# Performance work log

Hardware: AMD Instinct MI355X
Metric: run time of the kernel (lower is better)

Reference implementation:

```python
import jax, jax.numpy as jnp
import numpy as np

D = 256      # input_dim (object feature dim)
H = 256      # hidden_dim
N0 = 4096    # nodes in frame 0
N1 = 4096    # nodes in frame 1
E = 131072   # edges
MP_ITER = 3
LN_EPS = 1e-5


def _glorot(k, shape):
    return jax.random.normal(k, shape, jnp.float32) * (1.0 / np.sqrt(shape[0]))


def setup_inputs() -> dict:
    key = jax.random.key(0)
    ks = jax.random.split(key, 20)
    z = lambda n: jnp.zeros((n,), jnp.float32)
    o = lambda n: jnp.ones((n,), jnp.float32)
    return {
        'node0': jax.random.normal(ks[0], (N0, D), jnp.float32),
        'node1': jax.random.normal(ks[1], (N1, D), jnp.float32),
        'row': jax.random.randint(ks[2], (E,), 0, N0, jnp.int32),
        'col': jax.random.randint(ks[3], (E,), 0, N1, jnp.int32),
        # edge_mlp: Linear(2D,H) ReLU Linear(H,H) LN ReLU Linear(H,H)
        'e_w1': _glorot(ks[4], (2 * D, H)), 'e_b1': z(H),
        'e_w2': _glorot(ks[5], (H, H)),     'e_b2': z(H),
        'e_g': o(H), 'e_be': z(H),
        'e_w3': _glorot(ks[6], (H, H)),     'e_b3': z(H),
        # node_mlp: Linear(H+D,H) ReLU Linear(H,H) LN ReLU Linear(H,D)
        'n_w1': _glorot(ks[7], (H + D, H)), 'n_b1': z(H),
        'n_w2': _glorot(ks[8], (H, H)),     'n_b2': z(H),
        'n_g': o(H), 'n_be': z(H),
        'n_w3': _glorot(ks[9], (H, D)),     'n_b3': z(D),
        # edge_predictor: Linear(2D,H) ReLU Linear(H,1)
        'p_w1': _glorot(ks[10], (2 * D, H)), 'p_b1': z(H),
        'p_w2': _glorot(ks[11], (H, 1)),     'p_b2': z(1),
    }


def _ln(x, g, b):
    mu = jnp.mean(x, axis=-1, keepdims=True)
    var = jnp.mean(jnp.square(x - mu), axis=-1, keepdims=True)
    return (x - mu) * jax.lax.rsqrt(var + LN_EPS) * g + b


def reference(node0, node1, row, col,
              e_w1, e_b1, e_w2, e_b2, e_g, e_be, e_w3, e_b3,
              n_w1, n_b1, n_w2, n_b2, n_g, n_be, n_w3, n_b3,
              p_w1, p_b1, p_w2, p_b2):
    def edge_mlp(x):
        h = jax.nn.relu(x @ e_w1 + e_b1)
        h = _ln(h @ e_w2 + e_b2, e_g, e_be)
        return jax.nn.relu(h) @ e_w3 + e_b3

    def node_mlp(x):
        h = jax.nn.relu(x @ n_w1 + n_b1)
        h = _ln(h @ n_w2 + n_b2, n_g, n_be)
        return jax.nn.relu(h) @ n_w3 + n_b3

    for _ in range(MP_ITER):
        # gather -> edge MLP -> scatter-add -> node MLP (+ residual)
        e_in = jnp.concatenate([node0[row], node1[col]], axis=1)  # [E, 2D]
        edge_attr = edge_mlp(e_in)                                 # [E, H]
        agg = jax.ops.segment_sum(edge_attr, row, num_segments=node0.shape[0])  # [N0, H]
        node0 = node_mlp(jnp.concatenate([node0, agg], axis=1)) + node0

    pred_in = jnp.concatenate([node0[row], node1[col]], axis=1)   # [E, 2D]
    h = jax.nn.relu(pred_in @ p_w1 + p_b1)
    edge_preds = jax.nn.sigmoid(h @ p_w2 + p_b2)                   # [E, 1]
    return edge_preds
```

## Files before the change

### kernel.cpp

```cpp
#include <hip/hip_runtime.h>
#include <hip/hip_bf16.h>

#define NN0 4096
#define NEDGE 131072
#define NMP 3

typedef __attribute__((ext_vector_type(8))) short bf16x8;
typedef __attribute__((ext_vector_type(4))) float f32x4;

__device__ __forceinline__ unsigned short f2b(float v) {
  __hip_bfloat16 h = __float2bfloat16(v);
  return __builtin_bit_cast(unsigned short, h);
}

__device__ __forceinline__ float b2f(short s) {
  return __builtin_bit_cast(float, ((unsigned)(unsigned short)s) << 16);
}

__device__ __forceinline__ void gload_lds16(const void* g, void* l) {
  __builtin_amdgcn_global_load_lds(
      (const __attribute__((address_space(1))) void*)g,
      (__attribute__((address_space(3))) void*)l, 16, 0, 0);
}

#define MFMA(a, b, c) __builtin_amdgcn_mfma_f32_16x16x32_bf16((a), (b), (c), 0, 0, 0)

__device__ __forceinline__ void wfrag_body(const float* __restrict__ src,
                                           unsigned short* __restrict__ dst,
                                           int t, int C, int lgnkt) {
  const int j = t & 7;
  const int l = (t >> 3) & 63;
  const int rest = t >> 9;
  const int kt = rest & ((1 << lgnkt) - 1);
  const int ct = rest >> lgnkt;
  const int r = l & 15, q = l >> 4;
  const int k = (kt << 5) + (q << 3) + j;
  const int c = (ct << 4) + r;
  dst[t] = f2b(src[k * C + c]);
}

__global__ void prep_kernel(
    const float* e1, const float* e2, const float* e3,
    const float* n1, const float* n2, const float* n3, const float* p1,
    unsigned short* We1, unsigned short* We2, unsigned short* We3,
    unsigned short* Wn1, unsigned short* Wn2, unsigned short* Wn3,
    unsigned short* Wp1,
    const float* __restrict__ node0, const float* __restrict__ node1,
    unsigned short* __restrict__ n0b, float* __restrict__ n0f,
    unsigned short* __restrict__ n1b,
    const int* __restrict__ rowi, int* __restrict__ counts) {
  const int b = blockIdx.x;
  const int tid = threadIdx.x;
  if (b < 512)       wfrag_body(e1, We1, (b - 0) * 256 + tid, 256, 4);
  else if (b < 768)  wfrag_body(e2, We2, (b - 512) * 256 + tid, 256, 3);
  else if (b < 1024) wfrag_body(e3, We3, (b - 768) * 256 + tid, 256, 3);
  else if (b < 1536) wfrag_body(n1, Wn1, (b - 1024) * 256 + tid, 256, 4);
  else if (b < 1792) wfrag_body(n2, Wn2, (b - 1536) * 256 + tid, 256, 3);
  else if (b < 2048) wfrag_body(n3, Wn3, (b - 1792) * 256 + tid, 256, 3);
  else if (b < 2560) wfrag_body(p1, Wp1, (b - 2048) * 256 + tid, 256, 4);
  else {
    const int t = (b - 2560) * 256 + tid;
    const float a = node0[t], v = node1[t];
    n0b[t] = f2b(a);
    n0f[t] = a;
    n1b[t] = f2b(v);
    if (t < NEDGE) atomicAdd(&counts[rowi[t]], 1);
  }
}

__global__ void scan_kernel(const int* __restrict__ counts, int* __restrict__ pos) {
  __shared__ int part[256];
  const int t = threadIdx.x;
  const int base = t << 4;
  int local[16];
  int s = 0;
  #pragma unroll
  for (int i = 0; i < 16; ++i) { local[i] = s; s += counts[base + i]; }
  part[t] = s;
  __syncthreads();
  int val = s;
  #pragma unroll
  for (int off = 1; off < 256; off <<= 1) {
    const int add = (t >= off) ? part[t - off] : 0;
    __syncthreads();
    val += add;
    part[t] = val;
    __syncthreads();
  }
  const int excl = val - s;
  #pragma unroll
  for (int i = 0; i < 16; ++i) pos[base + i] = excl + local[i];
}

__global__ void fill_kernel(const int* __restrict__ rowi, int* __restrict__ pos,
                            int* __restrict__ perm) {
  const int e = blockIdx.x * 256 + threadIdx.x;
  if (e < NEDGE) {
    const int slot = atomicAdd(&pos[rowi[e]], 1);
    perm[slot] = e;
  }
}

__global__ __launch_bounds__(256, 2) void pre_gemm_kernel(
    const unsigned short* __restrict__ n0bA, const unsigned short* __restrict__ n1b,
    const unsigned short* __restrict__ We1, const unsigned short* __restrict__ Wp1,
    const float* __restrict__ e_b1,
    unsigned short* __restrict__ P0, unsigned short* __restrict__ P1,
    unsigned short* __restrict__ Pp1)
{
  __shared__ unsigned short smem[32 * 256];
  const int b = blockIdx.x;
  const int grp = b >> 7, mb = b & 127;
  const unsigned short* A;
  const unsigned short* W;
  int ktoff;
  const float* bias;
  unsigned short* out;
  if (grp == 0)      { A = n0bA; W = We1; ktoff = 0; bias = e_b1;    out = P0;  }
  else if (grp == 1) { A = n1b;  W = We1; ktoff = 8; bias = nullptr; out = P1;  }
  else               { A = n1b;  W = Wp1; ktoff = 8; bias = nullptr; out = Pp1; }

  const int tid = (int)threadIdx.x;
  const int ww = tid >> 6, l = tid & 63, r = l & 15, q = l >> 4;
  const int c0 = ww << 6;
  const int swz = (r & 7) << 4;

  #pragma unroll
  for (int s = 0; s < 4; ++s) {
    const int rp = (ww << 3) + (s << 1);
    const int row = rp + (l >> 5);
    const int g = (l & 31) ^ (row & 7);
    gload_lds16(A + (mb * 32 + row) * 256 + g * 8, &smem[rp * 256]);
  }
  __syncthreads();

  f32x4 acc[2][4];
  #pragma unroll
  for (int mt = 0; mt < 2; ++mt)
    #pragma unroll
    for (int nt = 0; nt < 4; ++nt)
      acc[mt][nt] = f32x4{0.f, 0.f, 0.f, 0.f};

  for (int ks = 0; ks < 8; ++ks) {
    bf16x8 a[2];
    #pragma unroll
    for (int mt = 0; mt < 2; ++mt)
      a[mt] = *(const bf16x8*)((const char*)smem + ((mt << 4) + r) * 512 +
                               (((ks << 6) | (q << 4)) ^ swz));
    #pragma unroll
    for (int nt = 0; nt < 4; ++nt) {
      bf16x8 bfr = *(const bf16x8*)(W + ((((ww << 2) + nt) << 4) + ktoff + ks) * 512 + (l << 3));
      #pragma unroll
      for (int mt = 0; mt < 2; ++mt)
        acc[mt][nt] = MFMA(a[mt], bfr, acc[mt][nt]);
    }
  }
  #pragma unroll
  for (int nt = 0; nt < 4; ++nt) {
    const int col = c0 + (nt << 4) + r;
    const float bv = bias ? bias[col] : 0.f;
    #pragma unroll
    for (int mt = 0; mt < 2; ++mt)
      #pragma unroll
      for (int i = 0; i < 4; ++i)
        out[(mb * 32 + (mt << 4) + (q << 2) + i) * 256 + col] = f2b(acc[mt][nt][i] + bv);
  }
}

__global__ __launch_bounds__(256, 2) void edge_mlp_kernel(
    const unsigned short* __restrict__ P0b, const unsigned short* __restrict__ P1b,
    const int* __restrict__ rowi, const int* __restrict__ coli,
    const int* __restrict__ perm,
    const unsigned short* __restrict__ W2, const float* __restrict__ b2,
    const float* __restrict__ lng, const float* __restrict__ lnb,
    float* __restrict__ S)
{
  __shared__ unsigned short smem[64 * 256];
  __shared__ float lnp[512];
  __shared__ int rs_s[64];
  __shared__ unsigned long long bmask_s;

  const int tid = (int)threadIdx.x;
  const int wn = tid >> 6, l = tid & 63, r = l & 15, q = l >> 4;
  const int bid = (int)blockIdx.x;
  const int swzb = ((bid & 7) << 8) + (bid >> 3);
  const int e0 = swzb * 64;
  const int c0 = wn << 6;
  const int swz = (r & 7) << 4;

  const int hrow = tid >> 2;
  const int cq = tid & 3;
  const int pe = perm[e0 + hrow];
  const int mrow = rowi[pe], mcol = coli[pe];
  if (cq == 0) rs_s[hrow] = mrow;
  const unsigned short* pu = P0b + mrow * 256;
  const unsigned short* pv = P1b + mcol * 256;
  const int hswz = (hrow & 7) << 4;

  #pragma unroll
  for (int jb = 0; jb < 2; ++jb) {
    bf16x8 uu[4], vv[4];
    #pragma unroll
    for (int j = 0; j < 4; ++j) {
      const int col0 = (cq << 6) + (jb << 5) + (j << 3);
      uu[j] = *(const bf16x8*)(pu + col0);
      vv[j] = *(const bf16x8*)(pv + col0);
    }
    #pragma unroll
    for (int j = 0; j < 4; ++j) {
      const int col0 = (cq << 6) + (jb << 5) + (j << 3);
      bf16x8 hpk;
      #pragma unroll
      for (int k = 0; k < 8; ++k)
        hpk[k] = (short)f2b(fmaxf(b2f(uu[j][k]) + b2f(vv[j][k]), 0.f));
      *(bf16x8*)((char*)smem + hrow * 512 + (((unsigned)(col0 * 2)) ^ hswz)) = hpk;
    }
  }
  __syncthreads();

  if (tid < 64) {
    const bool bnd = (tid == 63) || (rs_s[tid] != rs_s[tid + 1]);
    const unsigned long long m = __ballot(bnd);
    if (tid == 0) bmask_s = m;
  }

  f32x4 acc2[4][4];
  #pragma unroll
  for (int mt = 0; mt < 4; ++mt)
    #pragma unroll
    for (int nt = 0; nt < 4; ++nt)
      acc2[mt][nt] = f32x4{0.f, 0.f, 0.f, 0.f};
  __builtin_amdgcn_s_setprio(1);
  for (int ks = 0; ks < 8; ++ks) {
    bf16x8 a[4];
    #pragma unroll
    for (int mt = 0; mt < 4; ++mt)
      a[mt] = *(const bf16x8*)((const char*)smem + ((mt << 4) + r) * 512 +
                               (((ks << 6) | (q << 4)) ^ swz));
    #pragma unroll
    for (int nt = 0; nt < 4; ++nt) {
      bf16x8 b = *(const bf16x8*)(W2 + ((((wn << 2) + nt) << 3) + ks) * 512 + (l << 3));
      #pragma unroll
      for (int mt = 0; mt < 4; ++mt)
        acc2[mt][nt] = MFMA(a[mt], b, acc2[mt][nt]);
    }
  }
  __builtin_amdgcn_s_setprio(0);
  #pragma unroll
  for (int nt = 0; nt < 4; ++nt) {
    const float bias = b2[c0 + (nt << 4) + r];
    #pragma unroll
    for (int mt = 0; mt < 4; ++mt)
      #pragma unroll
      for (int i = 0; i < 4; ++i)
        acc2[mt][nt][i] += bias;
  }
  #pragma unroll
  for (int mt = 0; mt < 4; ++mt)
    #pragma unroll
    for (int i = 0; i < 4; ++i) {
      float s = 0.f, s2 = 0.f;
      #pragma unroll
      for (int nt = 0; nt < 4; ++nt) { const float x = acc2[mt][nt][i]; s += x; s2 += x * x; }
      #pragma unroll
      for (int m = 1; m < 16; m <<= 1) { s += __shfl_xor(s, m, 64); s2 += __shfl_xor(s2, m, 64); }
      if (r == 0) {
        const int rr = (mt << 4) + (q << 2) + i;
        lnp[(wn << 6) + rr] = s;
        lnp[256 + (wn << 6) + rr] = s2;
      }
    }
  __syncthreads();
  float mu[4][4], rstd[4][4];
  #pragma unroll
  for (int mt = 0; mt < 4; ++mt)
    #pragma unroll
    for (int i = 0; i < 4; ++i) {
      const int rr = (mt << 4) + (q << 2) + i;
      const float s  = lnp[rr] + lnp[64 + rr] + lnp[128 + rr] + lnp[192 + rr];
      const float s2 = lnp[256 + rr] + lnp[256 + 64 + rr] + lnp[256 + 128 + rr] + lnp[256 + 192 + rr];
      const float mean = s * (1.f / 256.f);
      const float var = s2 * (1.f / 256.f) - mean * mean;
      mu[mt][i] = mean;
      rstd[mt][i] = rsqrtf(var + 1e-5f);
    }
  #pragma unroll
  for (int nt = 0; nt < 4; ++nt) {
    const int hc = c0 + (nt << 4) + r;
    const float gv = lng[hc], bv = lnb[hc];
    #pragma unroll
    for (int mt = 0; mt < 4; ++mt)
      #pragma unroll
      for (int i = 0; i < 4; ++i) {
        const int hr = (mt << 4) + (q << 2) + i;
        const float x = fmaxf((acc2[mt][nt][i] - mu[mt][i]) * rstd[mt][i] * gv + bv, 0.f);
        *(unsigned short*)((char*)smem + hr * 512 + ((hc * 2) ^ ((hr & 7) << 4))) = f2b(x);
      }
  }
  __syncthreads();

  const unsigned long long bmask = bmask_s;
  const int cp = tid & 127;
  const int seg = tid >> 7;
  float s0 = 0.f, s1 = 0.f;
  #pragma unroll
  for (int j = 0; j < 32; ++j) {
    const int er = (seg << 5) + j;
    const unsigned v = *(const unsigned*)((const char*)smem + er * 512 +
                                          ((cp << 2) ^ ((er & 7) << 4)));
    s0 += b2f((short)(v & 0xffffu));
    s1 += b2f((short)(v >> 16));
    if (((bmask >> er) & 1ull) || (j == 31)) {
      float* dst = S + rs_s[er] * 256 + (cp << 1);
      atomicAdd(dst, s0);
      atomicAdd(dst + 1, s1);
      s0 = 0.f; s1 = 0.f;
    }
  }
}

__global__ __launch_bounds__(512, 2) void node_mlp_kernel(
    float* __restrict__ nf, float* __restrict__ S, const int* __restrict__ counts,
    const unsigned short* __restrict__ W1, const float* __restrict__ b1,
    const unsigned short* __restrict__ W2, const float* __restrict__ b2,
    const float* __restrict__ lng, const float* __restrict__ lnb,
    const unsigned short* __restrict__ W3, const float* __restrict__ b3,
    const unsigned short* __restrict__ We3, const float* __restrict__ e_b3,
    const unsigned short* __restrict__ We1, const float* __restrict__ e_b1,
    const unsigned short* __restrict__ Wp1, const float* __restrict__ p_b1,
    unsigned short* __restrict__ P0out, unsigned short* __restrict__ Pp0out)
{
  __shared__ unsigned short smem[16 * 512];
  __shared__ unsigned short Slds[16 * 256];
  __shared__ float lnp[256];
  const int tid = (int)threadIdx.x;
  const int ww = tid >> 6, l = tid & 63, r = l & 15, q = l >> 4;
  const int r0 = (int)blockIdx.x << 4;
  const int c0 = ww << 5;
  const int swz = (r & 7) << 4;

  {
    const int arow = tid >> 5;
    const int kc = tid & 31;
    const int nrow = r0 + arow;
    const int sw = (arow & 7) << 4;
    float v[16];
    if (kc < 16) {
      const float* src = nf + nrow * 256 + (kc << 4);
      *(f32x4*)(v + 0)  = *(const f32x4*)(src + 0);
      *(f32x4*)(v + 4)  = *(const f32x4*)(src + 4);
      *(f32x4*)(v + 8)  = *(const f32x4*)(src + 8);
      *(f32x4*)(v + 12) = *(const f32x4*)(src + 12);
      bf16x8 p0, p1;
      #pragma unroll
      for (int k = 0; k < 8; ++k) { p0[k] = (short)f2b(v[k]); p1[k] = (short)f2b(v[8 + k]); }
      const int base = arow * 1024;
      const int b0 = kc << 5;
      *(bf16x8*)((char*)smem + base + (b0 ^ sw)) = p0;
      *(bf16x8*)((char*)smem + base + ((b0 + 16) ^ sw)) = p1;
    } else {
      const int kc2 = kc - 16;
      float* src = S + nrow * 256 + (kc2 << 4);
      *(f32x4*)(v + 0)  = *(const f32x4*)(src + 0);
      *(f32x4*)(v + 4)  = *(const f32x4*)(src + 4);
      *(f32x4*)(v + 8)  = *(const f32x4*)(src + 8);
      *(f32x4*)(v + 12) = *(const f32x4*)(src + 12);
      *(f32x4*)(src + 0) = f32x4{0.f, 0.f, 0.f, 0.f};
      *(f32x4*)(src + 4) = f32x4{0.f, 0.f, 0.f, 0.f};
      *(f32x4*)(src + 8) = f32x4{0.f, 0.f, 0.f, 0.f};
      *(f32x4*)(src + 12) = f32x4{0.f, 0.f, 0.f, 0.f};
      bf16x8 p0, p1;
      #pragma unroll
      for (int k = 0; k < 8; ++k) { p0[k] = (short)f2b(v[k]); p1[k] = (short)f2b(v[8 + k]); }
      const int base = arow * 512;
      const int b0 = kc2 << 5;
      *(bf16x8*)((char*)Slds + base + (b0 ^ sw)) = p0;
      *(bf16x8*)((char*)Slds + base + ((b0 + 16) ^ sw)) = p1;
    }
  }
  __syncthreads();

  {
    f32x4 acc0[2];
    acc0[0] = f32x4{0.f, 0.f, 0.f, 0.f};
    acc0[1] = f32x4{0.f, 0.f, 0.f, 0.f};
    for (int ks = 0; ks < 8; ++ks) {
      bf16x8 a = *(const bf16x8*)((const char*)Slds + r * 512 + (((ks << 6) | (q << 4)) ^ swz));
      #pragma unroll
      for (int nt = 0; nt < 2; ++nt) {
        bf16x8 b = *(const bf16x8*)(We3 + ((((ww << 1) + nt) << 3) + ks) * 512 + (l << 3));
        acc0[nt] = MFMA(a, b, acc0[nt]);
      }
    }
    float degv[4];
    #pragma unroll
    for (int i = 0; i < 4; ++i) degv[i] = (float)counts[r0 + (q << 2) + i];
    #pragma unroll
    for (int nt = 0; nt < 2; ++nt) {
      const int col = c0 + (nt << 4) + r;
      const float bv = e_b3[col];
      #pragma unroll
      for (int i = 0; i < 4; ++i) {
        const int arow = (q << 2) + i;
        const float vv = acc0[nt][i] + degv[i] * bv;
        *(unsigned short*)((char*)smem + arow * 1024 +
                           (((512 + (col << 1))) ^ ((arow & 7) << 4))) = f2b(vv);
      }
    }
  }
  __syncthreads();

  f32x4 acc1[2];
  acc1[0] = f32x4{0.f, 0.f, 0.f, 0.f};
  acc1[1] = f32x4{0.f, 0.f, 0.f, 0.f};
  for (int ks = 0; ks < 16; ++ks) {
    bf16x8 a = *(const bf16x8*)((const char*)smem + r * 1024 + (((ks << 6) | (q << 4)) ^ swz));
    #pragma unroll
    for (int nt = 0; nt < 2; ++nt) {
      bf16x8 b = *(const bf16x8*)(W1 + ((((ww << 1) + nt) << 4) + ks) * 512 + (l << 3));
      acc1[nt] = MFMA(a, b, acc1[nt]);
    }
  }
  #pragma unroll
  for (int nt = 0; nt < 2; ++nt) {
    const float bias = b1[c0 + (nt << 4) + r];
    #pragma unroll
    for (int i = 0; i < 4; ++i) acc1[nt][i] = fmaxf(acc1[nt][i] + bias, 0.f);
  }
  __syncthreads();
  #pragma unroll
  for (int i = 0; i < 4; ++i) {
    const int hr = (q << 2) + i;
    const int hswz2 = (hr & 7) << 4;
    #pragma unroll
    for (int nt = 0; nt < 2; ++nt) {
      const int hc = c0 + (nt << 4) + r;
      *(unsigned short*)((char*)smem + hr * 512 + ((hc * 2) ^ hswz2)) = f2b(acc1[nt][i]);
    }
  }
  __syncthreads();

  f32x4 acc2[2];
  acc2[0] = f32x4{0.f, 0.f, 0.f, 0.f};
  acc2[1] = f32x4{0.f, 0.f, 0.f, 0.f};
  for (int ks = 0; ks < 8; ++ks) {
    bf16x8 a = *(const bf16x8*)((const char*)smem + r * 512 + (((ks << 6) | (q << 4)) ^ swz));
    #pragma unroll
    for (int nt = 0; nt < 2; ++nt) {
      bf16x8 b = *(const bf16x8*)(W2 + ((((ww << 1) + nt) << 3) + ks) * 512 + (l << 3));
      acc2[nt] = MFMA(a, b, acc2[nt]);
    }
  }
  #pragma unroll
  for (int nt = 0; nt < 2; ++nt) {
    const float bias = b2[c0 + (nt << 4) + r];
    #pragma unroll
    for (int i = 0; i < 4; ++i) acc2[nt][i] += bias;
  }
  #pragma unroll
  for (int i = 0; i < 4; ++i) {
    float s = acc2[0][i] + acc2[1][i];
    float s2 = acc2[0][i] * acc2[0][i] + acc2[1][i] * acc2[1][i];
    #pragma unroll
    for (int m = 1; m < 16; m <<= 1) { s += __shfl_xor(s, m, 64); s2 += __shfl_xor(s2, m, 64); }
    if (r == 0) {
      const int rr = (q << 2) + i;
      lnp[ww * 16 + rr] = s;
      lnp[128 + ww * 16 + rr] = s2;
    }
  }
  __syncthreads();
  float mu[4], rstd[4];
  #pragma unroll
  for (int i = 0; i < 4; ++i) {
    const int rr = (q << 2) + i;
    float s = 0.f, s2 = 0.f;
    #pragma unroll
    for (int w2i = 0; w2i < 8; ++w2i) { s += lnp[w2i * 16 + rr]; s2 += lnp[128 + w2i * 16 + rr]; }
    const float mean = s * (1.f / 256.f);
    const float var = s2 * (1.f / 256.f) - mean * mean;
    mu[i] = mean;
    rstd[i] = rsqrtf(var + 1e-5f);
  }
  #pragma unroll
  for (int nt = 0; nt < 2; ++nt) {
    const int hc = c0 + (nt << 4) + r;
    const float gv = lng[hc], bv = lnb[hc];
    #pragma unroll
    for (int i = 0; i < 4; ++i) {
      const int hr = (q << 2) + i;
      const float x = fmaxf((acc2[nt][i] - mu[i]) * rstd[i] * gv + bv, 0.f);
      *(unsigned short*)((char*)smem + hr * 512 + ((hc * 2) ^ ((hr & 7) << 4))) = f2b(x);
    }
  }
  __syncthreads();

  f32x4 acc3[2];
  acc3[0] = f32x4{0.f, 0.f, 0.f, 0.f};
  acc3[1] = f32x4{0.f, 0.f, 0.f, 0.f};
  for (int ks = 0; ks < 8; ++ks) {
    bf16x8 a = *(const bf16x8*)((const char*)smem + r * 512 + (((ks << 6) | (q << 4)) ^ swz));
    #pragma unroll
    for (int nt = 0; nt < 2; ++nt) {
      bf16x8 b = *(const bf16x8*)(W3 + ((((ww << 1) + nt) << 3) + ks) * 512 + (l << 3));
      acc3[nt] = MFMA(a, b, acc3[nt]);
    }
  }
  float y_loc[4][2];
  #pragma unroll
  for (int nt = 0; nt < 2; ++nt) {
    const float bias3 = b3[c0 + (nt << 4) + r];
    #pragma unroll
    for (int i = 0; i < 4; ++i) {
      const int nrow = r0 + (q << 2) + i;
      const int col = c0 + (nt << 4) + r;
      const float y = acc3[nt][i] + bias3 + nf[nrow * 256 + col];
      nf[nrow * 256 + col] = y;
      y_loc[i][nt] = y;
    }
  }
  __syncthreads();
  #pragma unroll
  for (int i = 0; i < 4; ++i) {
    const int hr = (q << 2) + i;
    const int hswz2 = (hr & 7) << 4;
    #pragma unroll
    for (int nt = 0; nt < 2; ++nt) {
      const int hc = c0 + (nt << 4) + r;
      *(unsigned short*)((char*)smem + hr * 512 + ((hc * 2) ^ hswz2)) = f2b(y_loc[i][nt]);
    }
  }
  __syncthreads();

  f32x4 acc4[2];
  acc4[0] = f32x4{0.f, 0.f, 0.f, 0.f};
  acc4[1] = f32x4{0.f, 0.f, 0.f, 0.f};
  for (int ks = 0; ks < 8; ++ks) {
    bf16x8 a = *(const bf16x8*)((const char*)smem + r * 512 + (((ks << 6) | (q << 4)) ^ swz));
    #pragma unroll
    for (int nt = 0; nt < 2; ++nt) {
      bf16x8 b = *(const bf16x8*)(We1 + ((((ww << 1) + nt) << 4) + ks) * 512 + (l << 3));
      acc4[nt] = MFMA(a, b, acc4[nt]);
    }
  }
  #pragma unroll
  for (int nt = 0; nt < 2; ++nt) {
    const int col = c0 + (nt << 4) + r;
    const float bv = e_b1[col];
    #pragma unroll
    for (int i = 0; i < 4; ++i)
      P0out[(r0 + (q << 2) + i) * 256 + col] = f2b(acc4[nt][i] + bv);
  }

  if (Pp0out != nullptr) {
    f32x4 acc5[2];
    acc5[0] = f32x4{0.f, 0.f, 0.f, 0.f};
    acc5[1] = f32x4{0.f, 0.f, 0.f, 0.f};
    for (int ks = 0; ks < 8; ++ks) {
      bf16x8 a = *(const bf16x8*)((const char*)smem + r * 512 + (((ks << 6) | (q << 4)) ^ swz));
      #pragma unroll
      for (int nt = 0; nt < 2; ++nt) {
        bf16x8 b = *(const bf16x8*)(Wp1 + ((((ww << 1) + nt) << 4) + ks) * 512 + (l << 3));
        acc5[nt] = MFMA(a, b, acc5[nt]);
      }
    }
    #pragma unroll
    for (int nt = 0; nt < 2; ++nt) {
      const int col = c0 + (nt << 4) + r;
      const float bv = p_b1[col];
      #pragma unroll
      for (int i = 0; i < 4; ++i)
        Pp0out[(r0 + (q << 2) + i) * 256 + col] = f2b(acc5[nt][i] + bv);
    }
  }
}

__global__ __launch_bounds__(256, 4) void pred_kernel(
    const unsigned short* __restrict__ Pp0, const unsigned short* __restrict__ Pp1,
    const int* __restrict__ rowi, const int* __restrict__ coli,
    const int* __restrict__ perm,
    const float* __restrict__ w2, const float* __restrict__ b2,
    float* __restrict__ out)
{
  const int g = (int)blockIdx.x * 256 + (int)threadIdx.x;
  const int e = perm[g];
  const int prow = rowi[e] * 256, pcol = coli[e] * 256;
  float acc = 0.f;
  #pragma unroll 4
  for (int j = 0; j < 32; ++j) {
    const bf16x8 u = *(const bf16x8*)(Pp0 + prow + (j << 3));
    const bf16x8 v = *(const bf16x8*)(Pp1 + pcol + (j << 3));
    #pragma unroll
    for (int k = 0; k < 8; ++k)
      acc += fmaxf(b2f(u[k]) + b2f(v[k]), 0.f) * w2[(j << 3) + k];
  }
  out[e] = 1.f / (1.f + expf(-(acc + b2[0])));
}

extern "C" void kernel_launch(void* const* d_in, const int* in_sizes, int n_in,
                              void* d_out, int out_size, void* d_ws, size_t ws_size,
                              hipStream_t stream) {
  const float* node0 = (const float*)d_in[0];
  const float* node1 = (const float*)d_in[1];
  const int* rowi = (const int*)d_in[2];
  const int* coli = (const int*)d_in[3];
  const float* e_w1 = (const float*)d_in[4];
  const float* e_b1 = (const float*)d_in[5];
  const float* e_w2 = (const float*)d_in[6];
  const float* e_b2 = (const float*)d_in[7];
  const float* e_g  = (const float*)d_in[8];
  const float* e_be = (const float*)d_in[9];
  const float* e_w3 = (const float*)d_in[10];
  const float* e_b3 = (const float*)d_in[11];
  const float* n_w1 = (const float*)d_in[12];
  const float* n_b1 = (const float*)d_in[13];
  const float* n_w2 = (const float*)d_in[14];
  const float* n_b2 = (const float*)d_in[15];
  const float* n_g  = (const float*)d_in[16];
  const float* n_be = (const float*)d_in[17];
  const float* n_w3 = (const float*)d_in[18];
  const float* n_b3 = (const float*)d_in[19];
  const float* p_w1 = (const float*)d_in[20];
  const float* p_b1 = (const float*)d_in[21];
  const float* p_w2 = (const float*)d_in[22];
  const float* p_b2 = (const float*)d_in[23];

  char* ws = (char*)d_ws;
  unsigned short* WTe1 = (unsigned short*)(ws + 0);
  unsigned short* WTe2 = (unsigned short*)(ws + 262144);
  unsigned short* WTe3 = (unsigned short*)(ws + 393216);
  unsigned short* WTn1 = (unsigned short*)(ws + 524288);
  unsigned short* WTn2 = (unsigned short*)(ws + 786432);
  unsigned short* WTn3 = (unsigned short*)(ws + 917504);
  unsigned short* WTp1 = (unsigned short*)(ws + 1048576);
  unsigned short* n1b  = (unsigned short*)(ws + 1310720);
  unsigned short* n0b  = (unsigned short*)(ws + 3407872);
  unsigned short* P0b  = (unsigned short*)(ws + 5505024);
  unsigned short* P1b  = (unsigned short*)(ws + 7602176);
  unsigned short* Pp0b = (unsigned short*)(ws + 9699328);
  unsigned short* Pp1b = (unsigned short*)(ws + 11796480);
  float* n0f  = (float*)(ws + 13893632);
  float* agg  = (float*)(ws + 18087936);
  int* perm   = (int*)(ws + 22282240);
  int* posb   = (int*)(ws + 22806528);
  int* counts = (int*)(ws + 22822912);

  hipMemsetAsync(counts, 0, 4096 * 4, stream);
  hipMemsetAsync(agg, 0, (size_t)NN0 * 256 * 4, stream);
  prep_kernel<<<6656, 256, 0, stream>>>(e_w1, e_w2, e_w3, n_w1, n_w2, n_w3, p_w1,
                                        WTe1, WTe2, WTe3, WTn1, WTn2, WTn3, WTp1,
                                        node0, node1, n0b, n0f, n1b, rowi, counts);
  scan_kernel<<<1, 256, 0, stream>>>(counts, posb);
  fill_kernel<<<512, 256, 0, stream>>>(rowi, posb, perm);

  pre_gemm_kernel<<<384, 256, 0, stream>>>(n0b, n1b, WTe1, WTp1, e_b1, P0b, P1b, Pp1b);

  for (int it = 0; it < NMP; ++it) {
    edge_mlp_kernel<<<NEDGE / 64, 256, 0, stream>>>(P0b, P1b, rowi, coli, perm,
        WTe2, e_b2, e_g, e_be, agg);
    node_mlp_kernel<<<NN0 / 16, 512, 0, stream>>>(n0f, agg, counts,
        WTn1, n_b1, WTn2, n_b2, n_g, n_be, WTn3, n_b3,
        WTe3, e_b3, WTe1, e_b1, WTp1, p_b1, P0b, (it == NMP - 1) ? Pp0b : nullptr);
  }
  pred_kernel<<<NEDGE / 256, 256, 0, stream>>>(Pp0b, Pp1b, rowi, coli, perm,
      p_w2, p_b2, (float*)d_out);
}
```

Measured before the change: 311.5 us.

## Segment-reduce edge MLP outputs in registers via shuffles instead of LDS staging

The edge kernel no longer writes the LayerNorm/ReLU outputs to shared memory and re-reads them for the scatter-add. Instead it keeps them in the accumulator registers, loops over segment boundaries from the bitmask, sums the rows of each segment with masked adds and cross-lane shuffles, and issues one atomic per column per segment. This removes an LDS round trip and a block barrier. In exchange it adds per-segment loop iterations with full masked reductions, and segments are now summed in fp32 rather than from values rounded to bf16.

Result: faster. 281.5 us (-9.6%).

```diff
diff --git a/kernel.cpp b/kernel.cpp
--- a/kernel.cpp
+++ b/kernel.cpp
@@ -291,31 +291,38 @@
     #pragma unroll
     for (int mt = 0; mt < 4; ++mt)
       #pragma unroll
-      for (int i = 0; i < 4; ++i) {
-        const int hr = (mt << 4) + (q << 2) + i;
-        const float x = fmaxf((acc2[mt][nt][i] - mu[mt][i]) * rstd[mt][i] * gv + bv, 0.f);
-        *(unsigned short*)((char*)smem + hr * 512 + ((hc * 2) ^ ((hr & 7) << 4))) = f2b(x);
-      }
-  }
-  __syncthreads();
-
-  const unsigned long long bmask = bmask_s;
-  const int cp = tid & 127;
-  const int seg = tid >> 7;
-  float s0 = 0.f, s1 = 0.f;
-  #pragma unroll
-  for (int j = 0; j < 32; ++j) {
-    const int er = (seg << 5) + j;
-    const unsigned v = *(const unsigned*)((const char*)smem + er * 512 +
-                                          ((cp << 2) ^ ((er & 7) << 4)));
-    s0 += b2f((short)(v & 0xffffu));
-    s1 += b2f((short)(v >> 16));
-    if (((bmask >> er) & 1ull) || (j == 31)) {
-      float* dst = S + rs_s[er] * 256 + (cp << 1);
-      atomicAdd(dst, s0);
-      atomicAdd(dst + 1, s1);
-      s0 = 0.f; s1 = 0.f;
-    }
+      for (int i = 0; i < 4; ++i)
+        acc2[mt][nt][i] = fmaxf((acc2[mt][nt][i] - mu[mt][i]) * rstd[mt][i] * gv + bv, 0.f);
+  }
+
+  unsigned long long m = bmask_s;
+  int a = 0;
+  while (m) {
+    const int bend = (int)__ffsll((long long)m);
+    float sseg[4];
+    #pragma unroll
+    for (int nt = 0; nt < 4; ++nt) {
+      float s = 0.f;
+      #pragma unroll
+      for (int mt = 0; mt < 4; ++mt)
+        #pragma unroll
+        for (int i = 0; i < 4; ++i) {
+          const int row = (mt << 4) + (q << 2) + i;
+          s += (row >= a && row < bend) ? acc2[mt][nt][i] : 0.f;
+        }
+      s += __shfl_xor(s, 16, 64);
+      s += __shfl_xor(s, 32, 64);
+      sseg[nt] = s;
+    }
+    if (q == 0) {
+      const int node = rs_s[bend - 1];
+      float* dst = S + node * 256 + c0 + r;
+      #pragma unroll
+      for (int nt = 0; nt < 4; ++nt)
+        atomicAdd(dst + (nt << 4), sseg[nt]);
+    }
+    a = bend;
+    m &= (m - 1);
   }
 }
 
```
